# Kernel optimization log

Hardware: AMD Instinct MI355X
Metric: run time of the kernel (lower is better)

## Reference

```python
import jax, jax.numpy as jnp
import numpy as np
import math

H = 5       # attention heads
DK = 20     # attdim // H
ATT = 100   # attdim
LAYERS = 2
B, L, BERT_DIM = 32, 256, 768


def _layernorm(x, a, b, eps=1e-6):
    mean = x.mean(-1, keepdims=True)
    std = jnp.std(x, axis=-1, ddof=1, keepdims=True)  # torch.std is unbiased
    return a * (x - mean) / (std + eps) + b


def _forward(sequence_output, src_mask, aspect_mask, short_mask,
             ln_a, ln_b, Wxx_w, Wxx_b, q_w, q_b, k_w, k_b,
             dense_w, dense_b, bias_m, W_w, W_b, Wx_w, Wx_b, clf_w, clf_b):
    Bn, Ln, _ = sequence_output.shape
    x = _layernorm(sequence_output, ln_a, ln_b)
    g = x @ Wxx_w + Wxx_b                                  # [B,L,100]
    asp_wn = aspect_mask.sum(1, keepdims=True)             # [B,1]
    aspect = (g * aspect_mask[..., None]).sum(1) / asp_wn  # [B,100]

    q = (g @ q_w + q_b).reshape(Bn, Ln, H, DK).transpose(0, 2, 1, 3)  # [B,H,L,dk]
    k = (g @ k_w + k_b).reshape(Bn, Ln, H, DK).transpose(0, 2, 1, 3)
    # aspect is expanded identically across heads/positions before dense -> [B,dk]
    asp = aspect @ dense_w + dense_b                       # [B,dk]
    scores = jnp.einsum('bhid,bhjd->bhij', q, k) / math.sqrt(DK)
    asp_sc = jnp.tanh(jnp.einsum('bd,bhjd->bhj', asp, k) + bias_m[0])
    scores = scores + asp_sc[:, :, None, :]
    scores = jnp.where(src_mask[:, None, None, :] == 0, -1e9, scores)
    scores = scores + short_mask                           # [B,1,L,L] broadcast
    adj = jax.nn.softmax(scores, axis=-1)                  # [B,H,L,L]

    # edge-update linear split so the [B,L,L,205] concat is never materialized:
    # edge[b,i,j] = adj_perm[b,i,j] @ Wa + go[b,j] @ W1 + go[b,i] @ W2 + b
    Wa, W1, W2 = Wx_w[:H], Wx_w[H:H + ATT], Wx_w[H + ATT:]
    go = g
    for i in range(LAYERS):
        # expand+matmul+mean over heads == mean-head message passing
        Ax = jnp.einsum('bhij,bjd->bid', adj, go) / H
        go = jax.nn.relu(Ax @ W_w + W_b)
        if i < LAYERS - 1:  # last edge update is discarded by the original output
            edge = (jnp.einsum('bhij,hk->bijk', adj, Wa)
                    + (go @ W1)[:, None, :, :]
                    + (go @ W2)[:, :, None, :]
                    + Wx_b)
            adj = edge.transpose(0, 3, 1, 2)
    # original: node_outputs = F.relu(gcn_outputs) (aggregate_W result is overwritten)
    h = jax.nn.relu(go)
    out1 = (h * aspect_mask[..., None]).sum(1) / asp_wn    # [B,100]
    return out1 @ clf_w + clf_b                            # [B,3]


def setup_inputs() -> dict:
    key = jax.random.key(0)
    ks = jax.random.split(key, 24)
    f32 = jnp.float32
    p = lambda k, shape, s=0.05: jax.random.normal(k, shape, dtype=f32) * s
    src_mask = jax.random.randint(ks[0], (B, L), 0, 2, dtype=jnp.int32).at[:, 0].set(1)
    aspect_mask = jnp.zeros((B, L), f32).at[:, 4:8].set(1.0)  # aspect span tokens
    return {
        'sequence_output': jax.random.normal(ks[1], (B, L, BERT_DIM), dtype=f32),
        'src_mask': src_mask,
        'aspect_mask': aspect_mask,
        'short_mask': p(ks[2], (B, 1, L, L), 1.0),
        'ln_a': jnp.ones((BERT_DIM,), f32),
        'ln_b': jnp.zeros((BERT_DIM,), f32),
        'Wxx_w': p(ks[3], (BERT_DIM, ATT)), 'Wxx_b': p(ks[4], (ATT,)),
        'q_w': p(ks[5], (ATT, ATT)), 'q_b': p(ks[6], (ATT,)),
        'k_w': p(ks[7], (ATT, ATT)), 'k_b': p(ks[8], (ATT,)),
        'dense_w': p(ks[9], (ATT, DK)), 'dense_b': p(ks[10], (DK,)),
        'bias_m': p(ks[11], (1,)),
        'W_w': p(ks[12], (ATT, ATT)), 'W_b': p(ks[13], (ATT,)),
        'Wx_w': p(ks[14], (H + 2 * ATT, H)), 'Wx_b': p(ks[15], (H,)),
        'clf_w': p(ks[16], (ATT, 3)), 'clf_b': p(ks[17], (3,)),
    }


def reference(sequence_output, src_mask, aspect_mask, short_mask,
              ln_a, ln_b, Wxx_w, Wxx_b, q_w, q_b, k_w, k_b,
              dense_w, dense_b, bias_m, W_w, W_b, Wx_w, Wx_b, clf_w, clf_b):
    return _forward(sequence_output, src_mask, aspect_mask, short_mask,
                    ln_a, ln_b, Wxx_w, Wxx_b, q_w, q_b, k_w, k_b,
                    dense_w, dense_b, bias_m, W_w, W_b, Wx_w, Wx_b, clf_w, clf_b)
```

## Files before the change

kernel.cpp:

```cpp
#include <hip/hip_runtime.h>
#include <math.h>

constexpr int CL = 256;
constexpr int CD = 768;
constexpr int CATT = 100;
constexpr int CH = 5;
constexpr int CDK = 20;

__device__ __forceinline__ void fma4(float4& a, float s, const float4& w) {
    a.x = fmaf(s, w.x, a.x);
    a.y = fmaf(s, w.y, a.y);
    a.z = fmaf(s, w.z, a.z);
    a.w = fmaf(s, w.w, a.w);
}

struct WPref { float4 r[7]; };
__device__ __forceinline__ void pref_load(WPref& p, const float4* __restrict__ src, int t) {
#pragma unroll
    for (int m = 0; m < 6; ++m) p.r[m] = src[t + 256 * m];
    if (t < 64) p.r[6] = src[t + 1536];
}
__device__ __forceinline__ void pref_store(const WPref& p, float* dst, int t) {
    float4* d4 = (float4*)dst;
#pragma unroll
    for (int m = 0; m < 6; ++m) d4[t + 256 * m] = p.r[m];
    if (t < 64) d4[t + 1536] = p.r[6];
}

__global__ __launch_bounds__(256) void k1_fused(
    const float* __restrict__ x, const float* __restrict__ ln_a,
    const float* __restrict__ ln_b, const float* __restrict__ Wxx_w,
    const float* __restrict__ Wxx_b, const float* __restrict__ q_w,
    const float* __restrict__ q_b, const float* __restrict__ k_w,
    const float* __restrict__ k_b, const float* __restrict__ amask,
    float* __restrict__ g, float* __restrict__ qt, float* __restrict__ ktb,
    float* __restrict__ aspect_raw)
{
    __shared__ float s_w[2][6400];
    __shared__ float s_xn[2][16 * 68];
    __shared__ float s_gt[16 * 100];
    __shared__ float s_mean[16], s_rinv[16];

    const int t = threadIdx.x;
    const int r0 = blockIdx.x * 16;
    const int wid = t >> 6, lane = t & 63;

    for (int rr = wid * 4; rr < wid * 4 + 4; ++rr) {
        const float* xr = x + (size_t)(r0 + rr) * CD;
        float xv[12];
        float s = 0.f;
#pragma unroll
        for (int m = 0; m < 12; ++m) { xv[m] = xr[lane + 64 * m]; s += xv[m]; }
#pragma unroll
        for (int o = 32; o; o >>= 1) s += __shfl_xor(s, o);
        float mean = s * (1.0f / 768.0f);
        float sq = 0.f;
#pragma unroll
        for (int m = 0; m < 12; ++m) { float d = xv[m] - mean; sq = fmaf(d, d, sq); }
#pragma unroll
        for (int o = 32; o; o >>= 1) sq += __shfl_xor(sq, o);
        if (lane == 0) {
            s_mean[rr] = mean;
            s_rinv[rr] = 1.0f / (sqrtf(sq * (1.0f / 767.0f)) + 1e-6f);
        }
    }

    const int cg = t % 25, rg = t / 25;
    const int c = cg * 4;
    const int xrow = t >> 4, xc4 = t & 15;
    const float* xrowp = x + (size_t)(r0 + xrow) * CD;

    WPref wp;
    pref_load(wp, (const float4*)Wxx_w, t);
    float4 xp = *(const float4*)(xrowp + xc4 * 4);
    float4 la = *(const float4*)(ln_a + xc4 * 4);
    float4 lb = *(const float4*)(ln_b + xc4 * 4);

    __syncthreads();

    float4 acc0 = make_float4(0.f, 0.f, 0.f, 0.f);
    float4 acc1 = make_float4(0.f, 0.f, 0.f, 0.f);

    for (int kt = 0; kt < 12; ++kt) {
        float* wbuf = s_w[kt & 1];
        float* xbuf = s_xn[kt & 1];
        {
            float mean = s_mean[xrow], rinv = s_rinv[xrow];
            float4 v;
            v.x = fmaf(la.x, (xp.x - mean) * rinv, lb.x);
            v.y = fmaf(la.y, (xp.y - mean) * rinv, lb.y);
            v.z = fmaf(la.z, (xp.z - mean) * rinv, lb.z);
            v.w = fmaf(la.w, (xp.w - mean) * rinv, lb.w);
            *(float4*)&xbuf[xrow * 68 + xc4 * 4] = v;
            pref_store(wp, wbuf, t);
        }
        if (kt < 11) {
            pref_load(wp, (const float4*)Wxx_w + (size_t)(kt + 1) * 1600, t);
            int kb = (kt + 1) * 64 + xc4 * 4;
            xp = *(const float4*)(xrowp + kb);
            la = *(const float4*)(ln_a + kb);
            lb = *(const float4*)(ln_b + kb);
        }
        __syncthreads();
        if (t < 200) {
#pragma unroll 2
            for (int kk = 0; kk < 64; kk += 4) {
                float4 a0 = *(const float4*)&xbuf[(rg * 2 + 0) * 68 + kk];
                float4 a1 = *(const float4*)&xbuf[(rg * 2 + 1) * 68 + kk];
                float4 w0 = *(const float4*)&wbuf[(kk + 0) * 100 + c];
                float4 w1 = *(const float4*)&wbuf[(kk + 1) * 100 + c];
                float4 w2 = *(const float4*)&wbuf[(kk + 2) * 100 + c];
                float4 w3 = *(const float4*)&wbuf[(kk + 3) * 100 + c];
                fma4(acc0, a0.x, w0); fma4(acc0, a0.y, w1); fma4(acc0, a0.z, w2); fma4(acc0, a0.w, w3);
                fma4(acc1, a1.x, w0); fma4(acc1, a1.y, w1); fma4(acc1, a1.z, w2); fma4(acc1, a1.w, w3);
            }
        }
    }
    __syncthreads();

    if (t < 200) {
        float4 bias = *(const float4*)&Wxx_b[c];
        float4 rv0, rv1;
        rv0.x = acc0.x + bias.x; rv0.y = acc0.y + bias.y; rv0.z = acc0.z + bias.z; rv0.w = acc0.w + bias.w;
        rv1.x = acc1.x + bias.x; rv1.y = acc1.y + bias.y; rv1.z = acc1.z + bias.z; rv1.w = acc1.w + bias.w;
        float4 rv[2] = { rv0, rv1 };
#pragma unroll
        for (int q = 0; q < 2; ++q) {
            int row = r0 + rg * 2 + q;
            *(float4*)&g[(size_t)row * CATT + c] = rv[q];
            *(float4*)&s_gt[(rg * 2 + q) * 100 + c] = rv[q];
            float m = amask[row];
            if (m != 0.f) {
                int b = row >> 8;
                atomicAdd(&aspect_raw[b * CATT + c + 0], m * rv[q].x);
                atomicAdd(&aspect_raw[b * CATT + c + 1], m * rv[q].y);
                atomicAdd(&aspect_raw[b * CATT + c + 2], m * rv[q].z);
                atomicAdd(&aspect_raw[b * CATT + c + 3], m * rv[q].w);
            }
        }
    }

    float* swf = &s_w[0][0];
    for (int pass = 0; pass < 2; ++pass) {
        const float4* ws4 = (const float4*)(pass ? k_w : q_w);
        for (int i = t; i < 2500; i += 256) ((float4*)swf)[i] = ws4[i];
        __syncthreads();
        if (t < 200) {
            const float* bb = pass ? k_b : q_b;
            float* outp = pass ? ktb : qt;
            float4 b0 = make_float4(0.f, 0.f, 0.f, 0.f);
            float4 b1 = make_float4(0.f, 0.f, 0.f, 0.f);
#pragma unroll 2
            for (int k = 0; k < 100; k += 4) {
                float4 a0 = *(const float4*)&s_gt[(rg * 2 + 0) * 100 + k];
                float4 a1 = *(const float4*)&s_gt[(rg * 2 + 1) * 100 + k];
                float4 w0 = *(const float4*)&swf[(k + 0) * 100 + c];
                float4 w1 = *(const float4*)&swf[(k + 1) * 100 + c];
                float4 w2 = *(const float4*)&swf[(k + 2) * 100 + c];
                float4 w3 = *(const float4*)&swf[(k + 3) * 100 + c];
                fma4(b0, a0.x, w0); fma4(b0, a0.y, w1); fma4(b0, a0.z, w2); fma4(b0, a0.w, w3);
                fma4(b1, a1.x, w0); fma4(b1, a1.y, w1); fma4(b1, a1.z, w2); fma4(b1, a1.w, w3);
            }
            float4 bias = *(const float4*)&bb[c];
            b0.x += bias.x; b0.y += bias.y; b0.z += bias.z; b0.w += bias.w;
            b1.x += bias.x; b1.y += bias.y; b1.z += bias.z; b1.w += bias.w;
            const int h = c / CDK, d = c % CDK;
            float4 rv[2] = { b0, b1 };
#pragma unroll
            for (int q = 0; q < 2; ++q) {
                int row = r0 + rg * 2 + q;
                int bidx = row >> 8, l = row & 255;
                *(float4*)&outp[((size_t)(bidx * CH + h) * CL + l) * CDK + d] = rv[q];
            }
        }
        __syncthreads();
    }
}

__global__ __launch_bounds__(256) void k45_attn_gcn0(
    const float* __restrict__ qt, const float* __restrict__ ktb,
    const float* __restrict__ aspect_raw, const float* __restrict__ amask,
    const float* __restrict__ dense_w, const float* __restrict__ dense_b,
    const float* __restrict__ bias_m, const int* __restrict__ src_mask,
    const float* __restrict__ shortm, const float* __restrict__ Wx_w,
    const float* __restrict__ g, const float* __restrict__ W_w,
    const float* __restrict__ W_b, float* __restrict__ adjW,
    float* __restrict__ go1, float* __restrict__ t1, float* __restrict__ t2,
    float* __restrict__ gW2S)
{
    constexpr int ICH = 16;
    __shared__ float s_pool[16 * 260];
    __shared__ float s_w[2][6400];
    __shared__ float s_q[CH * 320];
    __shared__ float s_red[CH][64];
    __shared__ float s_was[5];
    __shared__ float s_aspb[20];
    __shared__ float s_w1[100], s_w2[100];
    __shared__ float s_g1row[16];

    const int b = blockIdx.x >> 4, ic = blockIdx.x & 15;
    const int i0 = ic * ICH;
    const int t = threadIdx.x, lane = t & 63, wid = t >> 6;
    const int j = t;

    if (t < 5) {
        float s = 0.f;
        for (int k2 = 0; k2 < 5; ++k2) s += Wx_w[t * 5 + k2];
        s_was[t] = s;
    }
    if (t < 100) {
        float a = 0.f, c2 = 0.f;
#pragma unroll
        for (int h = 0; h < 5; ++h) {
            a += Wx_w[(5 + t) * 5 + h];
            c2 += Wx_w[(105 + t) * 5 + h];
        }
        s_w1[t] = a; s_w2[t] = c2;
    }
    float wn = 0.f;
    if (t < 64) {
        float4 mv = ((const float4*)amask)[b * 64 + t];
        wn = mv.x + mv.y + mv.z + mv.w;
#pragma unroll
        for (int o = 32; o; o >>= 1) wn += __shfl_xor(wn, o);
    }
    if (t < 20) {
        float a = 0.f;
        for (int d = 0; d < CATT; ++d)
            a = fmaf(aspect_raw[b * CATT + d], dense_w[d * CDK + t], a);
        s_aspb[t] = a / wn + dense_b[t];
    }
    {
        const float* qbase = qt + (size_t)b * CH * CL * CDK + (size_t)i0 * CDK;
        for (int i = t; i < CH * 320; i += 256) {
            int h = i / 320, r = i % 320;
            s_q[i] = qbase[(size_t)h * CL * CDK + r];
        }
    }

    const bool masked = (src_mask[b * CL + j] == 0);
    const float bm = bias_m[0];
    const float rs20 = 0.223606797749978969f;

    float sm[ICH];
#pragma unroll
    for (int ii = 0; ii < ICH; ++ii)
        sm[ii] = shortm[(size_t)(b * CL + i0 + ii) * CL + j];

    float accS[ICH], accW[ICH];
#pragma unroll
    for (int ii = 0; ii < ICH; ++ii) { accS[ii] = 0.f; accW[ii] = 0.f; }

    __syncthreads();

    for (int h = 0; h < CH; ++h) {
        float4 kr[5];
        const float* kp = ktb + ((size_t)(b * CH + h) * CL + j) * CDK;
#pragma unroll
        for (int m = 0; m < 5; ++m) kr[m] = *(const float4*)(kp + 4 * m);
        const float was_h = s_was[h];
        float s = bm;
#pragma unroll
        for (int m = 0; m < 5; ++m) {
            s = fmaf(s_aspb[4 * m + 0], kr[m].x, s);
            s = fmaf(s_aspb[4 * m + 1], kr[m].y, s);
            s = fmaf(s_aspb[4 * m + 2], kr[m].z, s);
            s = fmaf(s_aspb[4 * m + 3], kr[m].w, s);
        }
        const float aspsc = tanhf(s);

        float pv[ICH];
#pragma unroll
        for (int ii = 0; ii < ICH; ++ii) {
            const float* qrow = &s_q[h * 320 + ii * CDK];
            float sc = 0.f;
#pragma unroll
            for (int m = 0; m < 5; ++m) {
                float4 q4 = *(const float4*)(qrow + 4 * m);
                sc = fmaf(q4.x, kr[m].x, sc);
                sc = fmaf(q4.y, kr[m].y, sc);
                sc = fmaf(q4.z, kr[m].z, sc);
                sc = fmaf(q4.w, kr[m].w, sc);
            }
            sc = fmaf(sc, rs20, aspsc) + sm[ii];
            float p = masked ? 0.f : __expf(sc);
            pv[ii] = p;
            float ssum = p;
#pragma unroll
            for (int o = 32; o; o >>= 1) ssum += __shfl_xor(ssum, o);
            if (lane == 0) s_red[h][ii * 4 + wid] = ssum;
        }
        __syncthreads();
#pragma unroll
        for (int ii = 0; ii < ICH; ++ii) {
            float tot = s_red[h][ii * 4 + 0] + s_red[h][ii * 4 + 1] +
                        s_red[h][ii * 4 + 2] + s_red[h][ii * 4 + 3];
            float pn = pv[ii] * __frcp_rn(tot);
            accS[ii] += pn;
            accW[ii] = fmaf(was_h, pn, accW[ii]);
        }
    }

#pragma unroll
    for (int ii = 0; ii < ICH; ++ii) {
        adjW[(size_t)(b * CL + i0 + ii) * CL + j] = accW[ii];
        s_pool[ii * 260 + j] = accS[ii];
    }

    const int cg = t % 25, rg = t / 25;
    const int c = cg * 4;
    WPref wp;
    pref_load(wp, (const float4*)g + (size_t)b * CL * 25, t);

    float4 acc0 = make_float4(0.f, 0.f, 0.f, 0.f);
    float4 acc1 = make_float4(0.f, 0.f, 0.f, 0.f);
    for (int jt = 0; jt < 4; ++jt) {
        float* wbuf = s_w[jt & 1];
        pref_store(wp, wbuf, t);
        if (jt < 3)
            pref_load(wp, (const float4*)g + (size_t)(b * CL + (jt + 1) * 64) * 25, t);
        __syncthreads();
        if (t < 200) {
#pragma unroll 2
            for (int kk = 0; kk < 64; kk += 4) {
                float4 a0 = *(const float4*)&s_pool[(rg * 2 + 0) * 260 + jt * 64 + kk];
                float4 a1 = *(const float4*)&s_pool[(rg * 2 + 1) * 260 + jt * 64 + kk];
                float4 w0 = *(const float4*)&wbuf[(kk + 0) * 100 + c];
                float4 w1 = *(const float4*)&wbuf[(kk + 1) * 100 + c];
                float4 w2 = *(const float4*)&wbuf[(kk + 2) * 100 + c];
                float4 w3 = *(const float4*)&wbuf[(kk + 3) * 100 + c];
                fma4(acc0, a0.x, w0); fma4(acc0, a0.y, w1); fma4(acc0, a0.z, w2); fma4(acc0, a0.w, w3);
                fma4(acc1, a1.x, w0); fma4(acc1, a1.y, w1); fma4(acc1, a1.z, w2); fma4(acc1, a1.w, w3);
            }
        }
    }
    __syncthreads();

    float* s_ax = s_pool;
    if (t < 200) {
        float4 r;
        r.x = acc0.x * 0.2f; r.y = acc0.y * 0.2f; r.z = acc0.z * 0.2f; r.w = acc0.w * 0.2f;
        *(float4*)&s_ax[(rg * 2 + 0) * 108 + c] = r;
        r.x = acc1.x * 0.2f; r.y = acc1.y * 0.2f; r.z = acc1.z * 0.2f; r.w = acc1.w * 0.2f;
        *(float4*)&s_ax[(rg * 2 + 1) * 108 + c] = r;
    }
    float* swf = &s_w[0][0];
    {
        const float4* ws4 = (const float4*)W_w;
        for (int i = t; i < 2500; i += 256) ((float4*)swf)[i] = ws4[i];
    }
    __syncthreads();

    float4 o0 = make_float4(0.f, 0.f, 0.f, 0.f);
    float4 o1 = make_float4(0.f, 0.f, 0.f, 0.f);
    if (t < 200) {
#pragma unroll 2
        for (int k = 0; k < 100; k += 4) {
            float4 a0 = *(const float4*)&s_ax[(rg * 2 + 0) * 108 + k];
            float4 a1 = *(const float4*)&s_ax[(rg * 2 + 1) * 108 + k];
            float4 w0 = *(const float4*)&swf[(k + 0) * 100 + c];
            float4 w1 = *(const float4*)&swf[(k + 1) * 100 + c];
            float4 w2 = *(const float4*)&swf[(k + 2) * 100 + c];
            float4 w3 = *(const float4*)&swf[(k + 3) * 100 + c];
            fma4(o0, a0.x, w0); fma4(o0, a0.y, w1); fma4(o0, a0.z, w2); fma4(o0, a0.w, w3);
            fma4(o1, a1.x, w0); fma4(o1, a1.y, w1); fma4(o1, a1.z, w2); fma4(o1, a1.w, w3);
        }
        float4 bias = *(const float4*)&W_b[c];
        o0.x = fmaxf(o0.x + bias.x, 0.f); o0.y = fmaxf(o0.y + bias.y, 0.f);
        o0.z = fmaxf(o0.z + bias.z, 0.f); o0.w = fmaxf(o0.w + bias.w, 0.f);
        o1.x = fmaxf(o1.x + bias.x, 0.f); o1.y = fmaxf(o1.y + bias.y, 0.f);
        o1.z = fmaxf(o1.z + bias.z, 0.f); o1.w = fmaxf(o1.w + bias.w, 0.f);
        *(float4*)&go1[(size_t)(b * CL + i0 + rg * 2 + 0) * CATT + c] = o0;
        *(float4*)&go1[(size_t)(b * CL + i0 + rg * 2 + 1) * CATT + c] = o1;
    }
    float* s_go = s_pool + 1728;
    if (t < 200) {
        *(float4*)&s_go[(rg * 2 + 0) * 104 + c] = o0;
        *(float4*)&s_go[(rg * 2 + 1) * 104 + c] = o1;
    }
    __syncthreads();

    if (t < 128) {
        int r = t >> 3, seg = t & 7;
        int e0 = seg * 13, e1 = e0 + 13 < 100 ? e0 + 13 : 100;
        float a = 0.f, c2 = 0.f;
        for (int e = e0; e < e1; ++e) {
            float v = s_go[r * 104 + e];
            a = fmaf(v, s_w1[e], a);
            c2 = fmaf(v, s_w2[e], c2);
        }
        a += __shfl_xor(a, 1); a += __shfl_xor(a, 2); a += __shfl_xor(a, 4);
        c2 += __shfl_xor(c2, 1); c2 += __shfl_xor(c2, 2); c2 += __shfl_xor(c2, 4);
        if (seg == 0) {
            s_g1row[r] = a;
            gW2S[b * CL + i0 + r] = c2;
        }
    }
    __syncthreads();

    if (t < 100) {
        float a = 0.f, s2 = 0.f;
#pragma unroll
        for (int r = 0; r < 16; ++r) {
            float v = s_go[r * 104 + t];
            a = fmaf(s_g1row[r], v, a);
            s2 += v;
        }
        atomicAdd(&t1[b * CATT + t], a);
        atomicAdd(&t2[b * CATT + t], s2);
    }
}

__global__ __launch_bounds__(256) void k7_gcn1(
    const float* __restrict__ adjW, const float* __restrict__ go1,
    const float* __restrict__ W_w, const float* __restrict__ W_b,
    const float* __restrict__ t1, const float* __restrict__ t2,
    const float* __restrict__ gW2S, const float* __restrict__ Wx_b,
    const float* __restrict__ amask, float* __restrict__ out1_raw)
{
    __shared__ float s_pool[16 * 260];
    __shared__ float s_w[2][6400];
    const int b = blockIdx.x >> 4, ic = blockIdx.x & 15;
    const int i0 = ic * 16;
    const int t = threadIdx.x;

    {
        const float4* asrc = (const float4*)adjW + (size_t)(b * CL + i0) * 64;
#pragma unroll
        for (int m = 0; m < 4; ++m) {
            int i = t + 256 * m;
            int row = i >> 6, c4 = i & 63;
            *(float4*)&s_pool[row * 260 + c4 * 4] = asrc[i];
        }
    }

    const int cg = t % 25, rg = t / 25;
    const int c = cg * 4;
    WPref wp;
    pref_load(wp, (const float4*)go1 + (size_t)b * CL * 25, t);

    float4 acc0 = make_float4(0.f, 0.f, 0.f, 0.f);
    float4 acc1 = make_float4(0.f, 0.f, 0.f, 0.f);
    for (int jt = 0; jt < 4; ++jt) {
        float* wbuf = s_w[jt & 1];
        pref_store(wp, wbuf, t);
        if (jt < 3)
            pref_load(wp, (const float4*)go1 + (size_t)(b * CL + (jt + 1) * 64) * 25, t);
        __syncthreads();
        if (t < 200) {
#pragma unroll 2
            for (int kk = 0; kk < 64; kk += 4) {
                float4 a0 = *(const float4*)&s_pool[(rg * 2 + 0) * 260 + jt * 64 + kk];
                float4 a1 = *(const float4*)&s_pool[(rg * 2 + 1) * 260 + jt * 64 + kk];
                float4 w0 = *(const float4*)&wbuf[(kk + 0) * 100 + c];
                float4 w1 = *(const float4*)&wbuf[(kk + 1) * 100 + c];
                float4 w2 = *(const float4*)&wbuf[(kk + 2) * 100 + c];
                float4 w3 = *(const float4*)&wbuf[(kk + 3) * 100 + c];
                fma4(acc0, a0.x, w0); fma4(acc0, a0.y, w1); fma4(acc0, a0.z, w2); fma4(acc0, a0.w, w3);
                fma4(acc1, a1.x, w0); fma4(acc1, a1.y, w1); fma4(acc1, a1.z, w2); fma4(acc1, a1.w, w3);
            }
        }
    }
    __syncthreads();

    float* s_ax = s_pool;
    if (t < 200) {
        float wxbs = Wx_b[0] + Wx_b[1] + Wx_b[2] + Wx_b[3] + Wx_b[4];
        float4 t1v = *(const float4*)&t1[b * CATT + c];
        float4 t2v = *(const float4*)&t2[b * CATT + c];
        float gw0 = gW2S[b * CL + i0 + rg * 2 + 0] + wxbs;
        float gw1 = gW2S[b * CL + i0 + rg * 2 + 1] + wxbs;
        float4 r;
        r.x = (acc0.x + t1v.x + gw0 * t2v.x) * 0.2f;
        r.y = (acc0.y + t1v.y + gw0 * t2v.y) * 0.2f;
        r.z = (acc0.z + t1v.z + gw0 * t2v.z) * 0.2f;
        r.w = (acc0.w + t1v.w + gw0 * t2v.w) * 0.2f;
        *(float4*)&s_ax[(rg * 2 + 0) * 108 + c] = r;
        r.x = (acc1.x + t1v.x + gw1 * t2v.x) * 0.2f;
        r.y = (acc1.y + t1v.y + gw1 * t2v.y) * 0.2f;
        r.z = (acc1.z + t1v.z + gw1 * t2v.z) * 0.2f;
        r.w = (acc1.w + t1v.w + gw1 * t2v.w) * 0.2f;
        *(float4*)&s_ax[(rg * 2 + 1) * 108 + c] = r;
    }
    float* swf = &s_w[0][0];
    {
        const float4* ws4 = (const float4*)W_w;
        for (int i = t; i < 2500; i += 256) ((float4*)swf)[i] = ws4[i];
    }
    __syncthreads();

    if (t < 200) {
        float4 o0 = make_float4(0.f, 0.f, 0.f, 0.f);
        float4 o1 = make_float4(0.f, 0.f, 0.f, 0.f);
#pragma unroll 2
        for (int k = 0; k < 100; k += 4) {
            float4 a0 = *(const float4*)&s_ax[(rg * 2 + 0) * 108 + k];
            float4 a1 = *(const float4*)&s_ax[(rg * 2 + 1) * 108 + k];
            float4 w0 = *(const float4*)&swf[(k + 0) * 100 + c];
            float4 w1 = *(const float4*)&swf[(k + 1) * 100 + c];
            float4 w2 = *(const float4*)&swf[(k + 2) * 100 + c];
            float4 w3 = *(const float4*)&swf[(k + 3) * 100 + c];
            fma4(o0, a0.x, w0); fma4(o0, a0.y, w1); fma4(o0, a0.z, w2); fma4(o0, a0.w, w3);
            fma4(o1, a1.x, w0); fma4(o1, a1.y, w1); fma4(o1, a1.z, w2); fma4(o1, a1.w, w3);
        }
        float4 bias = *(const float4*)&W_b[c];
        o0.x = fmaxf(o0.x + bias.x, 0.f); o0.y = fmaxf(o0.y + bias.y, 0.f);
        o0.z = fmaxf(o0.z + bias.z, 0.f); o0.w = fmaxf(o0.w + bias.w, 0.f);
        o1.x = fmaxf(o1.x + bias.x, 0.f); o1.y = fmaxf(o1.y + bias.y, 0.f);
        o1.z = fmaxf(o1.z + bias.z, 0.f); o1.w = fmaxf(o1.w + bias.w, 0.f);
        float4 ov[2] = { o0, o1 };
#pragma unroll
        for (int q = 0; q < 2; ++q) {
            int row = b * CL + i0 + rg * 2 + q;
            float m = amask[row];
            if (m != 0.f) {
                atomicAdd(&out1_raw[b * CATT + c + 0], m * ov[q].x);
                atomicAdd(&out1_raw[b * CATT + c + 1], m * ov[q].y);
                atomicAdd(&out1_raw[b * CATT + c + 2], m * ov[q].z);
                atomicAdd(&out1_raw[b * CATT + c + 3], m * ov[q].w);
            }
        }
    }
}

__global__ __launch_bounds__(64) void k8_small(
    const float* __restrict__ out1_raw, const float* __restrict__ amask,
    const float* __restrict__ clf_w, const float* __restrict__ clf_b,
    float* __restrict__ out)
{
    const int b = blockIdx.x, t = threadIdx.x;
    float4 mv = ((const float4*)amask)[b * 64 + t];
    float wn = mv.x + mv.y + mv.z + mv.w;
#pragma unroll
    for (int o = 32; o; o >>= 1) wn += __shfl_xor(wn, o);
    if (t < 3) {
        float rwn = 1.f / wn;
        float a = clf_b[t];
        for (int d = 0; d < CATT; ++d)
            a = fmaf(out1_raw[b * CATT + d] * rwn, clf_w[d * 3 + t], a);
        out[b * 3 + t] = a;
    }
}

extern "C" void kernel_launch(void* const* d_in, const int* in_sizes, int n_in,
                              void* d_out, int out_size, void* d_ws, size_t ws_size,
                              hipStream_t stream) {
    const float* seq     = (const float*)d_in[0];
    const int*   srcm    = (const int*)d_in[1];
    const float* amask   = (const float*)d_in[2];
    const float* shortm  = (const float*)d_in[3];
    const float* ln_a    = (const float*)d_in[4];
    const float* ln_b    = (const float*)d_in[5];
    const float* Wxx_w   = (const float*)d_in[6];
    const float* Wxx_b   = (const float*)d_in[7];
    const float* q_w     = (const float*)d_in[8];
    const float* q_b     = (const float*)d_in[9];
    const float* k_w     = (const float*)d_in[10];
    const float* k_b     = (const float*)d_in[11];
    const float* dense_w = (const float*)d_in[12];
    const float* dense_b = (const float*)d_in[13];
    const float* bias_m  = (const float*)d_in[14];
    const float* W_w     = (const float*)d_in[15];
    const float* W_b     = (const float*)d_in[16];
    const float* Wx_w    = (const float*)d_in[17];
    const float* Wx_b    = (const float*)d_in[18];
    const float* clf_w   = (const float*)d_in[19];
    const float* clf_b   = (const float*)d_in[20];
    float* out = (float*)d_out;

    float* ws         = (float*)d_ws;
    float* g          = ws;
    float* qt         = g + 819200;
    float* ktb        = qt + 819200;
    float* go1        = ktb + 819200;
    float* adjW       = go1 + 819200;
    float* aspect_raw = adjW + 2097152;
    float* t1         = aspect_raw + 3200;
    float* t2         = t1 + 3200;
    float* out1_raw   = t2 + 3200;
    float* gW2S       = out1_raw + 3200;

    hipMemsetAsync(aspect_raw, 0, 4 * 3200 * sizeof(float), stream);
    hipLaunchKernelGGL(k1_fused, dim3(512), dim3(256), 0, stream, seq, ln_a, ln_b,
                       Wxx_w, Wxx_b, q_w, q_b, k_w, k_b, amask, g, qt, ktb, aspect_raw);
    hipLaunchKernelGGL(k45_attn_gcn0, dim3(512), dim3(256), 0, stream,
                       qt, ktb, aspect_raw, amask, dense_w, dense_b, bias_m, srcm,
                       shortm, Wx_w, g, W_w, W_b, adjW, go1, t1, t2, gW2S);
    hipLaunchKernelGGL(k7_gcn1, dim3(512), dim3(256), 0, stream,
                       adjW, go1, W_w, W_b, t1, t2, gW2S, Wx_b, amask, out1_raw);
    hipLaunchKernelGGL(k8_small, dim3(32), dim3(64), 0, stream,
                       out1_raw, amask, clf_w, clf_b, out);
}
```

Before: 280.0 us.

## Halve shared-memory weight tiles and software-pipeline loads to raise occupancy

Shrinks the double-buffered weight tiles in three kernels from 6400 to 3200 floats each and adds __launch_bounds__(256,3). The goal is to fit three blocks per CU. The K-loops are restructured so global loads for the next tile are issued before computing on the current tile, with one barrier per iteration. The q/k and W projections are also chunked into 20-row tiles so they overlap with loads instead of bulk-loading full weights. The cost is more, smaller iterations with more barriers, and possible register pressure from the occupancy bound.

```diff
diff --git a/kernel.cpp b/kernel.cpp
--- a/kernel.cpp
+++ b/kernel.cpp
@@ -14,20 +14,7 @@
     a.w = fmaf(s, w.w, a.w);
 }
 
-struct WPref { float4 r[7]; };
-__device__ __forceinline__ void pref_load(WPref& p, const float4* __restrict__ src, int t) {
-#pragma unroll
-    for (int m = 0; m < 6; ++m) p.r[m] = src[t + 256 * m];
-    if (t < 64) p.r[6] = src[t + 1536];
-}
-__device__ __forceinline__ void pref_store(const WPref& p, float* dst, int t) {
-    float4* d4 = (float4*)dst;
-#pragma unroll
-    for (int m = 0; m < 6; ++m) d4[t + 256 * m] = p.r[m];
-    if (t < 64) d4[t + 1536] = p.r[6];
-}
-
-__global__ __launch_bounds__(256) void k1_fused(
+__global__ __launch_bounds__(256, 3) void k1_fused(
     const float* __restrict__ x, const float* __restrict__ ln_a,
     const float* __restrict__ ln_b, const float* __restrict__ Wxx_w,
     const float* __restrict__ Wxx_b, const float* __restrict__ q_w,
@@ -36,14 +23,20 @@
     float* __restrict__ g, float* __restrict__ qt, float* __restrict__ ktb,
     float* __restrict__ aspect_raw)
 {
-    __shared__ float s_w[2][6400];
-    __shared__ float s_xn[2][16 * 68];
+    __shared__ float s_w[2][3200];
+    __shared__ float s_xn[2][16 * 36];
     __shared__ float s_gt[16 * 100];
+    __shared__ float s_ln[1536];
     __shared__ float s_mean[16], s_rinv[16];
 
     const int t = threadIdx.x;
     const int r0 = blockIdx.x * 16;
     const int wid = t >> 6, lane = t & 63;
+
+    if (t < 192) {
+        ((float4*)s_ln)[t] = ((const float4*)ln_a)[t];
+        ((float4*)(s_ln + 768))[t] = ((const float4*)ln_b)[t];
+    }
 
     for (int rr = wid * 4; rr < wid * 4 + 4; ++rr) {
         const float* xr = x + (size_t)(r0 + rr) * CD;
@@ -65,58 +58,66 @@
         }
     }
 
+    const float4* wsrc = (const float4*)Wxx_w;
+    float4 w0 = wsrc[t], w1 = wsrc[t + 256], w2 = wsrc[t + 512], w3;
+    if (t < 32) w3 = wsrc[t + 768];
+    const int rA = t >> 5, cA = t & 31;
+    float xa = x[(size_t)(r0 + rA) * CD + cA];
+    float xb = x[(size_t)(r0 + rA + 8) * CD + cA];
+
+    __syncthreads();
+
+    {
+        float4* d4 = (float4*)s_w[0];
+        d4[t] = w0; d4[t + 256] = w1; d4[t + 512] = w2;
+        if (t < 32) d4[t + 768] = w3;
+        float la = s_ln[cA], lbv = s_ln[768 + cA];
+        s_xn[0][rA * 36 + cA] = fmaf(la, (xa - s_mean[rA]) * s_rinv[rA], lbv);
+        s_xn[0][(rA + 8) * 36 + cA] = fmaf(la, (xb - s_mean[rA + 8]) * s_rinv[rA + 8], lbv);
+    }
+    __syncthreads();
+
     const int cg = t % 25, rg = t / 25;
     const int c = cg * 4;
-    const int xrow = t >> 4, xc4 = t & 15;
-    const float* xrowp = x + (size_t)(r0 + xrow) * CD;
-
-    WPref wp;
-    pref_load(wp, (const float4*)Wxx_w, t);
-    float4 xp = *(const float4*)(xrowp + xc4 * 4);
-    float4 la = *(const float4*)(ln_a + xc4 * 4);
-    float4 lb = *(const float4*)(ln_b + xc4 * 4);
-
-    __syncthreads();
-
     float4 acc0 = make_float4(0.f, 0.f, 0.f, 0.f);
     float4 acc1 = make_float4(0.f, 0.f, 0.f, 0.f);
 
-    for (int kt = 0; kt < 12; ++kt) {
-        float* wbuf = s_w[kt & 1];
-        float* xbuf = s_xn[kt & 1];
-        {
-            float mean = s_mean[xrow], rinv = s_rinv[xrow];
-            float4 v;
-            v.x = fmaf(la.x, (xp.x - mean) * rinv, lb.x);
-            v.y = fmaf(la.y, (xp.y - mean) * rinv, lb.y);
-            v.z = fmaf(la.z, (xp.z - mean) * rinv, lb.z);
-            v.w = fmaf(la.w, (xp.w - mean) * rinv, lb.w);
-            *(float4*)&xbuf[xrow * 68 + xc4 * 4] = v;
-            pref_store(wp, wbuf, t);
-        }
-        if (kt < 11) {
-            pref_load(wp, (const float4*)Wxx_w + (size_t)(kt + 1) * 1600, t);
-            int kb = (kt + 1) * 64 + xc4 * 4;
-            xp = *(const float4*)(xrowp + kb);
-            la = *(const float4*)(ln_a + kb);
-            lb = *(const float4*)(ln_b + kb);
+    for (int kt = 0; kt < 24; ++kt) {
+        if (kt < 23) {
+            const float4* ws = wsrc + (size_t)(kt + 1) * 800;
+            w0 = ws[t]; w1 = ws[t + 256]; w2 = ws[t + 512];
+            if (t < 32) w3 = ws[t + 768];
+            int gc = (kt + 1) * 32 + cA;
+            xa = x[(size_t)(r0 + rA) * CD + gc];
+            xb = x[(size_t)(r0 + rA + 8) * CD + gc];
+        }
+        if (t < 200) {
+            const float* wb = s_w[kt & 1];
+            const float* xbuf = s_xn[kt & 1];
+#pragma unroll 2
+            for (int kk = 0; kk < 32; kk += 4) {
+                float4 a0 = *(const float4*)&xbuf[(rg * 2 + 0) * 36 + kk];
+                float4 a1 = *(const float4*)&xbuf[(rg * 2 + 1) * 36 + kk];
+                float4 v0 = *(const float4*)&wb[(kk + 0) * 100 + c];
+                float4 v1 = *(const float4*)&wb[(kk + 1) * 100 + c];
+                float4 v2 = *(const float4*)&wb[(kk + 2) * 100 + c];
+                float4 v3 = *(const float4*)&wb[(kk + 3) * 100 + c];
+                fma4(acc0, a0.x, v0); fma4(acc0, a0.y, v1); fma4(acc0, a0.z, v2); fma4(acc0, a0.w, v3);
+                fma4(acc1, a1.x, v0); fma4(acc1, a1.y, v1); fma4(acc1, a1.z, v2); fma4(acc1, a1.w, v3);
+            }
+        }
+        if (kt < 23) {
+            float4* d4 = (float4*)s_w[(kt + 1) & 1];
+            d4[t] = w0; d4[t + 256] = w1; d4[t + 512] = w2;
+            if (t < 32) d4[t + 768] = w3;
+            int gc = (kt + 1) * 32 + cA;
+            float la = s_ln[gc], lbv = s_ln[768 + gc];
+            float* xd = s_xn[(kt + 1) & 1];
+            xd[rA * 36 + cA] = fmaf(la, (xa - s_mean[rA]) * s_rinv[rA], lbv);
+            xd[(rA + 8) * 36 + cA] = fmaf(la, (xb - s_mean[rA + 8]) * s_rinv[rA + 8], lbv);
         }
         __syncthreads();
-        if (t < 200) {
-#pragma unroll 2
-            for (int kk = 0; kk < 64; kk += 4) {
-                float4 a0 = *(const float4*)&xbuf[(rg * 2 + 0) * 68 + kk];
-                float4 a1 = *(const float4*)&xbuf[(rg * 2 + 1) * 68 + kk];
-                float4 w0 = *(const float4*)&wbuf[(kk + 0) * 100 + c];
-                float4 w1 = *(const float4*)&wbuf[(kk + 1) * 100 + c];
-                float4 w2 = *(const float4*)&wbuf[(kk + 2) * 100 + c];
-                float4 w3 = *(const float4*)&wbuf[(kk + 3) * 100 + c];
-                fma4(acc0, a0.x, w0); fma4(acc0, a0.y, w1); fma4(acc0, a0.z, w2); fma4(acc0, a0.w, w3);
-                fma4(acc1, a1.x, w0); fma4(acc1, a1.y, w1); fma4(acc1, a1.z, w2); fma4(acc1, a1.w, w3);
-            }
-        }
-    }
-    __syncthreads();
+    }
 
     if (t < 200) {
         float4 bias = *(const float4*)&Wxx_b[c];
@@ -140,44 +141,66 @@
         }
     }
 
-    float* swf = &s_w[0][0];
-    for (int pass = 0; pass < 2; ++pass) {
-        const float4* ws4 = (const float4*)(pass ? k_w : q_w);
-        for (int i = t; i < 2500; i += 256) ((float4*)swf)[i] = ws4[i];
+    const float4* qw4 = (const float4*)q_w;
+    const float4* kw4 = (const float4*)k_w;
+    float4 sA = qw4[t], sB;
+    if (t < 244) sB = qw4[t + 256];
+    __syncthreads();
+    {
+        float4* d4 = (float4*)s_w[0];
+        d4[t] = sA; if (t < 244) d4[t + 256] = sB;
+    }
+    __syncthreads();
+
+    float4 p0 = make_float4(0.f, 0.f, 0.f, 0.f);
+    float4 p1 = make_float4(0.f, 0.f, 0.f, 0.f);
+    for (int tau = 0; tau < 10; ++tau) {
+        if (tau < 9) {
+            const float4* src = (tau + 1 < 5) ? qw4 + (size_t)(tau + 1) * 500
+                                              : kw4 + (size_t)(tau - 4) * 500;
+            sA = src[t]; if (t < 244) sB = src[t + 256];
+        }
+        if (t < 200) {
+            const float* wb = s_w[tau & 1];
+            const int kb = (tau % 5) * 20;
+#pragma unroll 2
+            for (int kk = 0; kk < 20; kk += 4) {
+                float4 a0 = *(const float4*)&s_gt[(rg * 2 + 0) * 100 + kb + kk];
+                float4 a1 = *(const float4*)&s_gt[(rg * 2 + 1) * 100 + kb + kk];
+                float4 v0 = *(const float4*)&wb[(kk + 0) * 100 + c];
+                float4 v1 = *(const float4*)&wb[(kk + 1) * 100 + c];
+                float4 v2 = *(const float4*)&wb[(kk + 2) * 100 + c];
+                float4 v3 = *(const float4*)&wb[(kk + 3) * 100 + c];
+                fma4(p0, a0.x, v0); fma4(p0, a0.y, v1); fma4(p0, a0.z, v2); fma4(p0, a0.w, v3);
+                fma4(p1, a1.x, v0); fma4(p1, a1.y, v1); fma4(p1, a1.z, v2); fma4(p1, a1.w, v3);
+            }
+            if (tau == 4 || tau == 9) {
+                const float* bb = (tau == 4) ? q_b : k_b;
+                float* outp = (tau == 4) ? qt : ktb;
+                float4 bias = *(const float4*)&bb[c];
+                p0.x += bias.x; p0.y += bias.y; p0.z += bias.z; p0.w += bias.w;
+                p1.x += bias.x; p1.y += bias.y; p1.z += bias.z; p1.w += bias.w;
+                const int h = c / CDK, d = c % CDK;
+                float4 rv[2] = { p0, p1 };
+#pragma unroll
+                for (int q = 0; q < 2; ++q) {
+                    int row = r0 + rg * 2 + q;
+                    int bidx = row >> 8, l = row & 255;
+                    *(float4*)&outp[((size_t)(bidx * CH + h) * CL + l) * CDK + d] = rv[q];
+                }
+                p0 = make_float4(0.f, 0.f, 0.f, 0.f);
+                p1 = make_float4(0.f, 0.f, 0.f, 0.f);
+            }
+        }
+        if (tau < 9) {
+            float4* d4 = (float4*)s_w[(tau + 1) & 1];
+            d4[t] = sA; if (t < 244) d4[t + 256] = sB;
+        }
         __syncthreads();
-        if (t < 200) {
-            const float* bb = pass ? k_b : q_b;
-            float* outp = pass ? ktb : qt;
-            float4 b0 = make_float4(0.f, 0.f, 0.f, 0.f);
-            float4 b1 = make_float4(0.f, 0.f, 0.f, 0.f);
-#pragma unroll 2
-            for (int k = 0; k < 100; k += 4) {
-                float4 a0 = *(const float4*)&s_gt[(rg * 2 + 0) * 100 + k];
-                float4 a1 = *(const float4*)&s_gt[(rg * 2 + 1) * 100 + k];
-                float4 w0 = *(const float4*)&swf[(k + 0) * 100 + c];
-                float4 w1 = *(const float4*)&swf[(k + 1) * 100 + c];
-                float4 w2 = *(const float4*)&swf[(k + 2) * 100 + c];
-                float4 w3 = *(const float4*)&swf[(k + 3) * 100 + c];
-                fma4(b0, a0.x, w0); fma4(b0, a0.y, w1); fma4(b0, a0.z, w2); fma4(b0, a0.w, w3);
-                fma4(b1, a1.x, w0); fma4(b1, a1.y, w1); fma4(b1, a1.z, w2); fma4(b1, a1.w, w3);
-            }
-            float4 bias = *(const float4*)&bb[c];
-            b0.x += bias.x; b0.y += bias.y; b0.z += bias.z; b0.w += bias.w;
-            b1.x += bias.x; b1.y += bias.y; b1.z += bias.z; b1.w += bias.w;
-            const int h = c / CDK, d = c % CDK;
-            float4 rv[2] = { b0, b1 };
-#pragma unroll
-            for (int q = 0; q < 2; ++q) {
-                int row = r0 + rg * 2 + q;
-                int bidx = row >> 8, l = row & 255;
-                *(float4*)&outp[((size_t)(bidx * CH + h) * CL + l) * CDK + d] = rv[q];
-            }
-        }
-        __syncthreads();
     }
 }
 
-__global__ __launch_bounds__(256) void k45_attn_gcn0(
+__global__ __launch_bounds__(256, 3) void k45_attn_gcn0(
     const float* __restrict__ qt, const float* __restrict__ ktb,
     const float* __restrict__ aspect_raw, const float* __restrict__ amask,
     const float* __restrict__ dense_w, const float* __restrict__ dense_b,
@@ -190,7 +213,7 @@
 {
     constexpr int ICH = 16;
     __shared__ float s_pool[16 * 260];
-    __shared__ float s_w[2][6400];
+    __shared__ float s_w[2][3200];
     __shared__ float s_q[CH * 320];
     __shared__ float s_red[CH][64];
     __shared__ float s_was[5];
@@ -309,32 +332,45 @@
 
     const int cg = t % 25, rg = t / 25;
     const int c = cg * 4;
-    WPref wp;
-    pref_load(wp, (const float4*)g + (size_t)b * CL * 25, t);
+    const float4* g4 = (const float4*)g + (size_t)b * 6400;
+    float4 sA = g4[t], sB = g4[t + 256], sC = g4[t + 512], sD;
+    if (t < 32) sD = g4[t + 768];
+    {
+        float4* d4 = (float4*)s_w[0];
+        d4[t] = sA; d4[t + 256] = sB; d4[t + 512] = sC;
+        if (t < 32) d4[t + 768] = sD;
+    }
+    __syncthreads();
 
     float4 acc0 = make_float4(0.f, 0.f, 0.f, 0.f);
     float4 acc1 = make_float4(0.f, 0.f, 0.f, 0.f);
-    for (int jt = 0; jt < 4; ++jt) {
-        float* wbuf = s_w[jt & 1];
-        pref_store(wp, wbuf, t);
-        if (jt < 3)
-            pref_load(wp, (const float4*)g + (size_t)(b * CL + (jt + 1) * 64) * 25, t);
+    for (int jt = 0; jt < 8; ++jt) {
+        if (jt < 7) {
+            const float4* src = g4 + (size_t)(jt + 1) * 800;
+            sA = src[t]; sB = src[t + 256]; sC = src[t + 512];
+            if (t < 32) sD = src[t + 768];
+        }
+        if (t < 200) {
+            const float* wb = s_w[jt & 1];
+#pragma unroll 2
+            for (int kk = 0; kk < 32; kk += 4) {
+                float4 a0 = *(const float4*)&s_pool[(rg * 2 + 0) * 260 + jt * 32 + kk];
+                float4 a1 = *(const float4*)&s_pool[(rg * 2 + 1) * 260 + jt * 32 + kk];
+                float4 v0 = *(const float4*)&wb[(kk + 0) * 100 + c];
+                float4 v1 = *(const float4*)&wb[(kk + 1) * 100 + c];
+                float4 v2 = *(const float4*)&wb[(kk + 2) * 100 + c];
+                float4 v3 = *(const float4*)&wb[(kk + 3) * 100 + c];
+                fma4(acc0, a0.x, v0); fma4(acc0, a0.y, v1); fma4(acc0, a0.z, v2); fma4(acc0, a0.w, v3);
+                fma4(acc1, a1.x, v0); fma4(acc1, a1.y, v1); fma4(acc1, a1.z, v2); fma4(acc1, a1.w, v3);
+            }
+        }
+        if (jt < 7) {
+            float4* d4 = (float4*)s_w[(jt + 1) & 1];
+            d4[t] = sA; d4[t + 256] = sB; d4[t + 512] = sC;
+            if (t < 32) d4[t + 768] = sD;
+        }
         __syncthreads();
-        if (t < 200) {
-#pragma unroll 2
-            for (int kk = 0; kk < 64; kk += 4) {
-                float4 a0 = *(const float4*)&s_pool[(rg * 2 + 0) * 260 + jt * 64 + kk];
-                float4 a1 = *(const float4*)&s_pool[(rg * 2 + 1) * 260 + jt * 64 + kk];
-                float4 w0 = *(const float4*)&wbuf[(kk + 0) * 100 + c];
-                float4 w1 = *(const float4*)&wbuf[(kk + 1) * 100 + c];
-                float4 w2 = *(const float4*)&wbuf[(kk + 2) * 100 + c];
-                float4 w3 = *(const float4*)&wbuf[(kk + 3) * 100 + c];
-                fma4(acc0, a0.x, w0); fma4(acc0, a0.y, w1); fma4(acc0, a0.z, w2); fma4(acc0, a0.w, w3);
-                fma4(acc1, a1.x, w0); fma4(acc1, a1.y, w1); fma4(acc1, a1.z, w2); fma4(acc1, a1.w, w3);
-            }
-        }
-    }
-    __syncthreads();
+    }
 
     float* s_ax = s_pool;
     if (t < 200) {
@@ -344,27 +380,45 @@
         r.x = acc1.x * 0.2f; r.y = acc1.y * 0.2f; r.z = acc1.z * 0.2f; r.w = acc1.w * 0.2f;
         *(float4*)&s_ax[(rg * 2 + 1) * 108 + c] = r;
     }
-    float* swf = &s_w[0][0];
-    {
-        const float4* ws4 = (const float4*)W_w;
-        for (int i = t; i < 2500; i += 256) ((float4*)swf)[i] = ws4[i];
+    const float4* ww4 = (const float4*)W_w;
+    sA = ww4[t]; if (t < 244) sB = ww4[t + 256];
+    {
+        float4* d4 = (float4*)s_w[0];
+        d4[t] = sA; if (t < 244) d4[t + 256] = sB;
     }
     __syncthreads();
 
     float4 o0 = make_float4(0.f, 0.f, 0.f, 0.f);
     float4 o1 = make_float4(0.f, 0.f, 0.f, 0.f);
+    for (int wt = 0; wt < 5; ++wt) {
+        if (wt < 4) {
+            const float4* src = ww4 + (size_t)(wt + 1) * 500;
+            sA = src[t]; if (t < 244) sB = src[t + 256];
+        }
+        if (t < 200) {
+            const float* wb = s_w[wt & 1];
+            const int kb = wt * 20;
+#pragma unroll 2
+            for (int kk = 0; kk < 20; kk += 4) {
+                float4 a0 = *(const float4*)&s_ax[(rg * 2 + 0) * 108 + kb + kk];
+                float4 a1 = *(const float4*)&s_ax[(rg * 2 + 1) * 108 + kb + kk];
+                float4 v0 = *(const float4*)&wb[(kk + 0) * 100 + c];
+                float4 v1 = *(const float4*)&wb[(kk + 1) * 100 + c];
+                float4 v2 = *(const float4*)&wb[(kk + 2) * 100 + c];
+                float4 v3 = *(const float4*)&wb[(kk + 3) * 100 + c];
+                fma4(o0, a0.x, v0); fma4(o0, a0.y, v1); fma4(o0, a0.z, v2); fma4(o0, a0.w, v3);
+                fma4(o1, a1.x, v0); fma4(o1, a1.y, v1); fma4(o1, a1.z, v2); fma4(o1, a1.w, v3);
+            }
+        }
+        if (wt < 4) {
+            float4* d4 = (float4*)s_w[(wt + 1) & 1];
+            d4[t] = sA; if (t < 244) d4[t + 256] = sB;
+        }
+        __syncthreads();
+    }
+
+    float* s_go = s_pool + 1728;
     if (t < 200) {
-#pragma unroll 2
-        for (int k = 0; k < 100; k += 4) {
-            float4 a0 = *(const float4*)&s_ax[(rg * 2 + 0) * 108 + k];
-            float4 a1 = *(const float4*)&s_ax[(rg * 2 + 1) * 108 + k];
-            float4 w0 = *(const float4*)&swf[(k + 0) * 100 + c];
-            float4 w1 = *(const float4*)&swf[(k + 1) * 100 + c];
-            float4 w2 = *(const float4*)&swf[(k + 2) * 100 + c];
-            float4 w3 = *(const float4*)&swf[(k + 3) * 100 + c];
-            fma4(o0, a0.x, w0); fma4(o0, a0.y, w1); fma4(o0, a0.z, w2); fma4(o0, a0.w, w3);
-            fma4(o1, a1.x, w0); fma4(o1, a1.y, w1); fma4(o1, a1.z, w2); fma4(o1, a1.w, w3);
-        }
         float4 bias = *(const float4*)&W_b[c];
         o0.x = fmaxf(o0.x + bias.x, 0.f); o0.y = fmaxf(o0.y + bias.y, 0.f);
         o0.z = fmaxf(o0.z + bias.z, 0.f); o0.w = fmaxf(o0.w + bias.w, 0.f);
@@ -372,9 +426,6 @@
         o1.z = fmaxf(o1.z + bias.z, 0.f); o1.w = fmaxf(o1.w + bias.w, 0.f);
         *(float4*)&go1[(size_t)(b * CL + i0 + rg * 2 + 0) * CATT + c] = o0;
         *(float4*)&go1[(size_t)(b * CL + i0 + rg * 2 + 1) * CATT + c] = o1;
-    }
-    float* s_go = s_pool + 1728;
-    if (t < 200) {
         *(float4*)&s_go[(rg * 2 + 0) * 104 + c] = o0;
         *(float4*)&s_go[(rg * 2 + 1) * 104 + c] = o1;
     }
@@ -411,7 +462,7 @@
     }
 }
 
-__global__ __launch_bounds__(256) void k7_gcn1(
+__global__ __launch_bounds__(256, 3) void k7_gcn1(
     const float* __restrict__ adjW, const float* __restrict__ go1,
     const float* __restrict__ W_w, const float* __restrict__ W_b,
     const float* __restrict__ t1, const float* __restrict__ t2,
@@ -419,7 +470,7 @@
     const float* __restrict__ amask, float* __restrict__ out1_raw)
 {
     __shared__ float s_pool[16 * 260];
-    __shared__ float s_w[2][6400];
+    __shared__ float s_w[2][3200];
     const int b = blockIdx.x >> 4, ic = blockIdx.x & 15;
     const int i0 = ic * 16;
     const int t = threadIdx.x;
@@ -433,35 +484,47 @@
             *(float4*)&s_pool[row * 260 + c4 * 4] = asrc[i];
         }
     }
-
     const int cg = t % 25, rg = t / 25;
     const int c = cg * 4;
-    WPref wp;
-    pref_load(wp, (const float4*)go1 + (size_t)b * CL * 25, t);
+    const float4* g4 = (const float4*)go1 + (size_t)b * 6400;
+    float4 sA = g4[t], sB = g4[t + 256], sC = g4[t + 512], sD;
+    if (t < 32) sD = g4[t + 768];
+    {
+        float4* d4 = (float4*)s_w[0];
+        d4[t] = sA; d4[t + 256] = sB; d4[t + 512] = sC;
+        if (t < 32) d4[t + 768] = sD;
+    }
+    __syncthreads();
 
     float4 acc0 = make_float4(0.f, 0.f, 0.f, 0.f);
     float4 acc1 = make_float4(0.f, 0.f, 0.f, 0.f);
-    for (int jt = 0; jt < 4; ++jt) {
-        float* wbuf = s_w[jt & 1];
-        pref_store(wp, wbuf, t);
-        if (jt < 3)
-            pref_load(wp, (const float4*)go1 + (size_t)(b * CL + (jt + 1) * 64) * 25, t);
+    for (int jt = 0; jt < 8; ++jt) {
+        if (jt < 7) {
+            const float4* src = g4 + (size_t)(jt + 1) * 800;
+            sA = src[t]; sB = src[t + 256]; sC = src[t + 512];
+            if (t < 32) sD = src[t + 768];
+        }
+        if (t < 200) {
+            const float* wb = s_w[jt & 1];
+#pragma unroll 2
+            for (int kk = 0; kk < 32; kk += 4) {
+                float4 a0 = *(const float4*)&s_pool[(rg * 2 + 0) * 260 + jt * 32 + kk];
+                float4 a1 = *(const float4*)&s_pool[(rg * 2 + 1) * 260 + jt * 32 + kk];
+                float4 v0 = *(const float4*)&wb[(kk + 0) * 100 + c];
+                float4 v1 = *(const float4*)&wb[(kk + 1) * 100 + c];
+                float4 v2 = *(const float4*)&wb[(kk + 2) * 100 + c];
+                float4 v3 = *(const float4*)&wb[(kk + 3) * 100 + c];
+                fma4(acc0, a0.x, v0); fma4(acc0, a0.y, v1); fma4(acc0, a0.z, v2); fma4(acc0, a0.w, v3);
+                fma4(acc1, a1.x, v0); fma4(acc1, a1.y, v1); fma4(acc1, a1.z, v2); fma4(acc1, a1.w, v3);
+            }
+        }
+        if (jt < 7) {
+            float4* d4 = (float4*)s_w[(jt + 1) & 1];
+            d4[t] = sA; d4[t + 256] = sB; d4[t + 512] = sC;
+            if (t < 32) d4[t + 768] = sD;
+        }
         __syncthreads();
-        if (t < 200) {
-#pragma unroll 2
-            for (int kk = 0; kk < 64; kk += 4) {
-                float4 a0 = *(const float4*)&s_pool[(rg * 2 + 0) * 260 + jt * 64 + kk];
-                float4 a1 = *(const float4*)&s_pool[(rg * 2 + 1) * 260 + jt * 64 + kk];
-                float4 w0 = *(const float4*)&wbuf[(kk + 0) * 100 + c];
-                float4 w1 = *(const float4*)&wbuf[(kk + 1) * 100 + c];
-                float4 w2 = *(const float4*)&wbuf[(kk + 2) * 100 + c];
-                float4 w3 = *(const float4*)&wbuf[(kk + 3) * 100 + c];
-                fma4(acc0, a0.x, w0); fma4(acc0, a0.y, w1); fma4(acc0, a0.z, w2); fma4(acc0, a0.w, w3);
-                fma4(acc1, a1.x, w0); fma4(acc1, a1.y, w1); fma4(acc1, a1.z, w2); fma4(acc1, a1.w, w3);
-            }
-        }
-    }
-    __syncthreads();
+    }
 
     float* s_ax = s_pool;
     if (t < 200) {
@@ -482,27 +545,44 @@
         r.w = (acc1.w + t1v.w + gw1 * t2v.w) * 0.2f;
         *(float4*)&s_ax[(rg * 2 + 1) * 108 + c] = r;
     }
-    float* swf = &s_w[0][0];
-    {
-        const float4* ws4 = (const float4*)W_w;
-        for (int i = t; i < 2500; i += 256) ((float4*)swf)[i] = ws4[i];
-    }
-    __syncthreads();
+    const float4* ww4 = (const float4*)W_w;
+    sA = ww4[t]; if (t < 244) sB = ww4[t + 256];
+    {
+        float4* d4 = (float4*)s_w[0];
+        d4[t] = sA; if (t < 244) d4[t + 256] = sB;
+    }
+    __syncthreads();
+
+    float4 o0 = make_float4(0.f, 0.f, 0.f, 0.f);
+    float4 o1 = make_float4(0.f, 0.f, 0.f, 0.f);
+    for (int wt = 0; wt < 5; ++wt) {
+        if (wt < 4) {
+            const float4* src = ww4 + (size_t)(wt + 1) * 500;
+            sA = src[t]; if (t < 244) sB = src[t + 256];
+        }
+        if (t < 200) {
+            const float* wb = s_w[wt & 1];
+            const int kb = wt * 20;
+#pragma unroll 2
+            for (int kk = 0; kk < 20; kk += 4) {
+                float4 a0 = *(const float4*)&s_ax[(rg * 2 + 0) * 108 + kb + kk];
+                float4 a1 = *(const float4*)&s_ax[(rg * 2 + 1) * 108 + kb + kk];
+                float4 v0 = *(const float4*)&wb[(kk + 0) * 100 + c];
+                float4 v1 = *(const float4*)&wb[(kk + 1) * 100 + c];
+                float4 v2 = *(const float4*)&wb[(kk + 2) * 100 + c];
+                float4 v3 = *(const float4*)&wb[(kk + 3) * 100 + c];
+                fma4(o0, a0.x, v0); fma4(o0, a0.y, v1); fma4(o0, a0.z, v2); fma4(o0, a0.w, v3);
+                fma4(o1, a1.x, v0); fma4(o1, a1.y, v1); fma4(o1, a1.z, v2); fma4(o1, a1.w, v3);
+            }
+        }
+        if (wt < 4) {
+            float4* d4 = (float4*)s_w[(wt + 1) & 1];
+            d4[t] = sA; if (t < 244) d4[t + 256] = sB;
+        }
+        __syncthreads();
+    }
 
     if (t < 200) {
-        float4 o0 = make_float4(0.f, 0.f, 0.f, 0.f);
-        float4 o1 = make_float4(0.f, 0.f, 0.f, 0.f);
-#pragma unroll 2
-        for (int k = 0; k < 100; k += 4) {
-            float4 a0 = *(const float4*)&s_ax[(rg * 2 + 0) * 108 + k];
-            float4 a1 = *(const float4*)&s_ax[(rg * 2 + 1) * 108 + k];
-            float4 w0 = *(const float4*)&swf[(k + 0) * 100 + c];
-            float4 w1 = *(const float4*)&swf[(k + 1) * 100 + c];
-            float4 w2 = *(const float4*)&swf[(k + 2) * 100 + c];
-            float4 w3 = *(const float4*)&swf[(k + 3) * 100 + c];
-            fma4(o0, a0.x, w0); fma4(o0, a0.y, w1); fma4(o0, a0.z, w2); fma4(o0, a0.w, w3);
-            fma4(o1, a1.x, w0); fma4(o1, a1.y, w1); fma4(o1, a1.z, w2); fma4(o1, a1.w, w3);
-        }
         float4 bias = *(const float4*)&W_b[c];
         o0.x = fmaxf(o0.x + bias.x, 0.f); o0.y = fmaxf(o0.y + bias.y, 0.f);
         o0.z = fmaxf(o0.z + bias.z, 0.f); o0.w = fmaxf(o0.w + bias.w, 0.f);
```

Measured after the change: 241.8 us. 1.16x faster.
